# Kernel tuning notes

Hardware: AMD Instinct MI355X
Metric: run time of the kernel (lower is better)

## Reference

```python
import jax, jax.numpy as jnp
import numpy as np

DIM = 768
NUM_HEADS = 12
HEAD_DIM = DIM // NUM_HEADS
SCALE = HEAD_DIM ** -0.5


def setup_inputs() -> dict:
    key = jax.random.key(0)
    k1, k2, k3, k4 = jax.random.split(key, 4)
    B, N = 4, 2048
    x = jax.random.normal(k1, (B, N, DIM), dtype=jnp.float32)
    # torch Linear(dim, 3*dim, bias=False): weight [3*dim, dim]
    w_qkv = jax.random.normal(k2, (3 * DIM, DIM), dtype=jnp.float32) * (DIM ** -0.5)
    # proj: Linear(dim, dim) with bias
    w_proj = jax.random.normal(k3, (DIM, DIM), dtype=jnp.float32) * (DIM ** -0.5)
    b_proj = jax.random.normal(k4, (DIM,), dtype=jnp.float32) * 0.01
    return {"x": x, "w_qkv": w_qkv, "w_proj": w_proj, "b_proj": b_proj}


def reference(x, w_qkv, w_proj, b_proj):
    B, N, D = x.shape
    H, Hd = NUM_HEADS, HEAD_DIM
    qkv = x @ w_qkv.T                              # [B, N, 3D]
    qkv = qkv.reshape(B, N, 3, H, Hd)
    qkv = jnp.transpose(qkv, (2, 0, 3, 1, 4))      # [3, B, H, N, Hd]
    q, k, v = qkv[0], qkv[1], qkv[2]
    attn = jnp.einsum('bhnd,bhmd->bhnm', q, k) * SCALE  # [B, H, N, N]
    attn = jax.nn.softmax(attn, axis=-1)
    out = jnp.einsum('bhnm,bhmd->bhnd', attn, v)   # [B, H, N, Hd]
    out = jnp.transpose(out, (0, 2, 1, 3)).reshape(B, N, D)
    return out @ w_proj.T + b_proj
```

## Files before the change

kernel.cpp:

```cpp
#include <hip/hip_runtime.h>
#include <hip/hip_bf16.h>

#define DIM      768
#define NHEADS   12
#define HEADDIM  64
#define BATCH    4
#define SEQ      2048
#define NROWS    (BATCH * SEQ)
#define QKVCOLS  (3 * DIM)
#define SLOT     ((size_t)BATCH * NHEADS * SEQ * HEADDIM)

#define QSCALE_LOG2 0.18033688011112042f

typedef short bf16x8_t __attribute__((ext_vector_type(8)));
typedef short bf16x4_t __attribute__((ext_vector_type(4)));
typedef float f32x4_t  __attribute__((ext_vector_type(4)));

__device__ __forceinline__ short f2bf(float f) {
    union { __hip_bfloat16 h; short s; } u;
    u.h = __float2bfloat16(f);
    return u.s;
}

__device__ __forceinline__ float exp2_fast(float x) {
#if __has_builtin(__builtin_amdgcn_exp2f)
    return __builtin_amdgcn_exp2f(x);
#else
    return __expf(x * 0.6931471805599453f);
#endif
}

__device__ __forceinline__ void stage16(const __hip_bfloat16* g, __hip_bfloat16* l) {
    __builtin_amdgcn_global_load_lds(
        (const __attribute__((address_space(1))) void*)g,
        (__attribute__((address_space(3))) void*)l,
        16, 0, 0);
}

#define NX8  ((size_t)NROWS * DIM / 8)
#define NWQ8 ((size_t)QKVCOLS * DIM / 8)
#define NWP8 ((size_t)DIM * DIM / 8)

__global__ __launch_bounds__(256) void cvt_all(const float* __restrict__ X,
                                               const float* __restrict__ Wq,
                                               const float* __restrict__ Wp,
                                               __hip_bfloat16* __restrict__ Xb,
                                               __hip_bfloat16* __restrict__ Wqb,
                                               __hip_bfloat16* __restrict__ Wpb) {
    size_t i = (size_t)blockIdx.x * 256 + threadIdx.x;
    const float* src; __hip_bfloat16* dst; size_t off;
    if (i < NX8)                  { src = X;  dst = Xb;  off = i; }
    else if (i < NX8 + NWQ8)      { src = Wq; dst = Wqb; off = i - NX8; }
    else                          { src = Wp; dst = Wpb; off = i - NX8 - NWQ8; }
    float4 a = ((const float4*)src)[off * 2];
    float4 b = ((const float4*)src)[off * 2 + 1];
    bf16x8_t o;
    o[0] = f2bf(a.x); o[1] = f2bf(a.y); o[2] = f2bf(a.z); o[3] = f2bf(a.w);
    o[4] = f2bf(b.x); o[5] = f2bf(b.y); o[6] = f2bf(b.z); o[7] = f2bf(b.w);
    *(bf16x8_t*)(dst + off * 8) = o;
}

#define GEMM_CORE(Aptr, Bptr)                                                   \
    __shared__ __hip_bfloat16 As[128 * 64];                                     \
    __shared__ __hip_bfloat16 Bs[128 * 64];                                     \
    const int tid  = threadIdx.x;                                               \
    const int wave = tid >> 6;                                                  \
    const int lane = tid & 63;                                                  \
    const int quad = lane >> 4;                                                 \
    const int l16  = lane & 15;                                                 \
    const int wm   = wave >> 1;                                                 \
    const int wn   = wave & 1;                                                  \
    const int m0   = blockIdx.x * 128;                                          \
    const int n0   = blockIdx.y * 128;                                          \
    const int sr   = lane >> 3;                     \
    const int sc   = ((lane & 7) ^ sr) * 8;         \
    f32x4_t acc[4][4];                                                          \
    _Pragma("unroll")                                                           \
    for (int i = 0; i < 4; i++)                                                 \
        _Pragma("unroll")                                                       \
        for (int j = 0; j < 4; j++) acc[i][j] = (f32x4_t){0.f, 0.f, 0.f, 0.f};  \
    for (int k0 = 0; k0 < 768; k0 += 64) {                                      \
        __syncthreads();                                                        \
        _Pragma("unroll")                                                       \
        for (int i = 0; i < 4; i++) {                                           \
            int seg = wave * 4 + i;                                  \
            int row = seg * 8 + sr;                                             \
            stage16(Aptr + (size_t)(m0 + row) * 768 + k0 + sc, As + seg * 512); \
            stage16(Bptr + (size_t)(n0 + row) * 768 + k0 + sc, Bs + seg * 512); \
        }                                                                       \
        __syncthreads();               \
        _Pragma("unroll")                                                       \
        for (int kc = 0; kc < 2; kc++) {                                        \
            const int dsw = ((kc * 4 + quad) ^ (l16 & 7)) * 8;                  \
            bf16x8_t af[4], bfr[4];                                             \
            _Pragma("unroll")                                                   \
            for (int mt = 0; mt < 4; mt++)                                      \
                af[mt] = *(const bf16x8_t*)(As + (wm * 64 + mt * 16 + l16) * 64 + dsw); \
            _Pragma("unroll")                                                   \
            for (int nt = 0; nt < 4; nt++)                                      \
                bfr[nt] = *(const bf16x8_t*)(Bs + (wn * 64 + nt * 16 + l16) * 64 + dsw); \
            _Pragma("unroll")                                                   \
            for (int mt = 0; mt < 4; mt++)                                      \
                _Pragma("unroll")                                               \
                for (int nt = 0; nt < 4; nt++)                                  \
                    acc[mt][nt] = __builtin_amdgcn_mfma_f32_16x16x32_bf16(      \
                        af[mt], bfr[nt], acc[mt][nt], 0, 0, 0);                 \
        }                                                                       \
    }

__global__ __launch_bounds__(256) void qkv_gemm(const __hip_bfloat16* __restrict__ Wqb,
                                                const __hip_bfloat16* __restrict__ Xb,
                                                __hip_bfloat16* __restrict__ QKV) {
    GEMM_CORE(Wqb, Xb)

    const int bidx = n0 >> 11;
    const int nb   = (n0 & 2047) + wn * 64;
#pragma unroll
    for (int mt = 0; mt < 4; mt++) {
        int colbase = m0 + wm * 64 + mt * 16;
        int which   = colbase / 768;
        int rem     = colbase - which * 768;
        int h       = rem >> 6;
        int dbase   = (rem & 63) + quad * 4;
#pragma unroll
        for (int nt = 0; nt < 4; nt++) {
            int n = nb + nt * 16 + l16;
            if (which == 2) {
                size_t base = 2 * SLOT + (((size_t)bidx * NHEADS + h) * HEADDIM + dbase) * SEQ + n;
#pragma unroll
                for (int r = 0; r < 4; r++)
                    QKV[base + (size_t)r * SEQ] = __float2bfloat16(acc[mt][nt][r]);
            } else {
                float sc2 = (which == 0) ? QSCALE_LOG2 : 1.0f;
                size_t addr = (size_t)which * SLOT
                            + (((size_t)bidx * NHEADS + h) * SEQ + n) * HEADDIM + dbase;
                bf16x4_t pk;
#pragma unroll
                for (int r = 0; r < 4; r++) pk[r] = f2bf(acc[mt][nt][r] * sc2);
                *(bf16x4_t*)(QKV + addr) = pk;
            }
        }
    }
}

__global__ __launch_bounds__(512, 6) void attn(const __hip_bfloat16* __restrict__ QKV,
                                               __hip_bfloat16* __restrict__ ATT) {
    __shared__ __hip_bfloat16 lds[288 * 64];

    const int tid  = threadIdx.x;
    const int wave = tid >> 6;
    const int lane = tid & 63;
    const int quad = lane >> 4;
    const int l16  = lane & 15;
    const int qb   = blockIdx.x;
    const int bh   = blockIdx.y;
    const int b    = bh / NHEADS;
    const int h    = bh - b * NHEADS;

    const __hip_bfloat16* Qg = QKV + 0 * SLOT + (((size_t)b * NHEADS + h) * SEQ) * HEADDIM;
    const __hip_bfloat16* Kg = QKV + 1 * SLOT + (((size_t)b * NHEADS + h) * SEQ) * HEADDIM;
    const __hip_bfloat16* Vg = QKV + 2 * SLOT + (((size_t)b * NHEADS + h) * HEADDIM) * SEQ;

    const int rs = tid >> 3;
    const int es = (tid & 7) * 8;

#pragma unroll
    for (int i = 0; i < 2; i++) {
        int c = tid + i * 512;
        int r = c >> 3, e = (c & 7) * 8;
        *(bf16x8_t*)(lds + r * 72 + e) =
            *(const bf16x8_t*)(Qg + (size_t)(qb * 128 + r) * HEADDIM + e);
    }
    *(bf16x8_t*)(lds + 9216 + rs * 72 + es)  = *(const bf16x8_t*)(Kg + (size_t)rs * HEADDIM + es);
    *(bf16x8_t*)(lds + 13824 + rs * 72 + es) = *(const bf16x8_t*)(Vg + (size_t)rs * SEQ + es);
    __syncthreads();

    bf16x8_t aq[2];
#pragma unroll
    for (int kc = 0; kc < 2; kc++)
        aq[kc] = *(const bf16x8_t*)(lds + (wave * 16 + l16) * 72 + kc * 32 + quad * 8);
    __syncthreads();

    f32x4_t o[4];
#pragma unroll
    for (int dt = 0; dt < 4; dt++) o[dt] = (f32x4_t){0.f, 0.f, 0.f, 0.f};
    float l_part = 0.f;

    for (int t = 0; t < SEQ / 64; t++) {
        const int cur  = t & 1;
        const int boff = cur ? 0 : 9216;
        const __hip_bfloat16* Kc = lds + boff;
        const __hip_bfloat16* Vc = lds + boff + 4608;

        bf16x8_t nk, nv;
        const bool has_next = (t + 1 < SEQ / 64);
        if (has_next) {
            int nn0 = (t + 1) * 64;
            nk = *(const bf16x8_t*)(Kg + (size_t)(nn0 + rs) * HEADDIM + es);
            nv = *(const bf16x8_t*)(Vg + (size_t)rs * SEQ + nn0 + es);
        }

        f32x4_t s[4];
#pragma unroll
        for (int mt = 0; mt < 4; mt++) s[mt] = (f32x4_t){0.f, 0.f, 0.f, 0.f};
#pragma unroll
        for (int kc = 0; kc < 2; kc++) {
#pragma unroll
            for (int mt = 0; mt < 4; mt++) {
                bf16x8_t bk = *(const bf16x8_t*)(Kc + (mt * 16 + l16) * 72 + kc * 32 + quad * 8);
                s[mt] = __builtin_amdgcn_mfma_f32_16x16x32_bf16(bk, aq[kc], s[mt], 0, 0, 0);
            }
        }

#pragma unroll
        for (int mt = 0; mt < 4; mt++)
#pragma unroll
            for (int r = 0; r < 4; r++) {
                float p = exp2_fast(s[mt][r]);
                s[mt][r] = p;
                l_part += p;
            }

#pragma unroll
        for (int kb = 0; kb < 4; kb++) {
            bf16x4_t pb;
#pragma unroll
            for (int j = 0; j < 4; j++) pb[j] = f2bf(s[kb][j]);
#pragma unroll
            for (int dt = 0; dt < 4; dt++) {
                bf16x4_t av = *(const bf16x4_t*)(Vc + (dt * 16 + l16) * 72 + kb * 16 + quad * 4);
                o[dt] = __builtin_amdgcn_mfma_f32_16x16x16bf16_1k(av, pb, o[dt], 0, 0, 0);
            }
        }

        if (has_next) {
            const int aoff = cur ? 9216 : 0;
            *(bf16x8_t*)(lds + aoff + rs * 72 + es)        = nk;
            *(bf16x8_t*)(lds + aoff + 4608 + rs * 72 + es) = nv;
        }
        __syncthreads();
    }

    l_part += __shfl_xor(l_part, 16);
    l_part += __shfl_xor(l_part, 32);
    float inv = 1.f / l_part;

    const int n = qb * 128 + wave * 16 + l16;
    __hip_bfloat16* orow = ATT + ((size_t)b * SEQ + n) * DIM + h * HEADDIM + quad * 4;
#pragma unroll
    for (int dt = 0; dt < 4; dt++) {
        bf16x4_t pk;
#pragma unroll
        for (int r = 0; r < 4; r++) pk[r] = f2bf(o[dt][r] * inv);
        *(bf16x4_t*)(orow + dt * 16) = pk;
    }
}

__global__ __launch_bounds__(256) void proj_gemm(const __hip_bfloat16* __restrict__ A,
                                                 const __hip_bfloat16* __restrict__ B,
                                                 const float* __restrict__ bias,
                                                 float* __restrict__ OUT) {
    GEMM_CORE(A, B)

#pragma unroll
    for (int mt = 0; mt < 4; mt++) {
#pragma unroll
        for (int nt = 0; nt < 4; nt++) {
            int col = n0 + wn * 64 + nt * 16 + l16;
            float bv = bias[col];
#pragma unroll
            for (int r = 0; r < 4; r++) {
                int row = m0 + wm * 64 + mt * 16 + quad * 4 + r;
                OUT[(size_t)row * 768 + col] = acc[mt][nt][r] + bv;
            }
        }
    }
}

extern "C" void kernel_launch(void* const* d_in, const int* in_sizes, int n_in,
                              void* d_out, int out_size, void* d_ws, size_t ws_size,
                              hipStream_t stream) {
    const float* x      = (const float*)d_in[0];
    const float* w_qkv  = (const float*)d_in[1];
    const float* w_proj = (const float*)d_in[2];
    const float* b_proj = (const float*)d_in[3];
    float* out = (float*)d_out;

    __hip_bfloat16* qkv_ws = (__hip_bfloat16*)d_ws;
    __hip_bfloat16* xb     = qkv_ws + 3 * SLOT;
    __hip_bfloat16* att_ws = xb;
    __hip_bfloat16* wqb    = xb + (size_t)NROWS * DIM;
    __hip_bfloat16* wpb    = wqb + (size_t)QKVCOLS * DIM;

    int cvt_blocks = (int)((NX8 + NWQ8 + NWP8) / 256);
    cvt_all<<<cvt_blocks, 256, 0, stream>>>(x, w_qkv, w_proj, xb, wqb, wpb);

    dim3 g1(QKVCOLS / 128, NROWS / 128);
    qkv_gemm<<<g1, 256, 0, stream>>>(wqb, xb, qkv_ws);

    dim3 g2(SEQ / 128, BATCH * NHEADS);
    attn<<<g2, 512, 0, stream>>>(qkv_ws, att_ws);

    dim3 g3(NROWS / 128, DIM / 128);
    proj_gemm<<<g3, 256, 0, stream>>>(att_ws, wpb, b_proj, out);
}
```

Before: 237.7 us.

## Double-buffer GEMM LDS tiles and remap blocks to XCDs for L2 locality

```diff
diff --git a/kernel.cpp b/kernel.cpp
--- a/kernel.cpp
+++ b/kernel.cpp
@@ -61,8 +61,8 @@
 }
 
 #define GEMM_CORE(Aptr, Bptr)                                                   \
-    __shared__ __hip_bfloat16 As[128 * 64];                                     \
-    __shared__ __hip_bfloat16 Bs[128 * 64];                                     \
+    __shared__ __hip_bfloat16 As[2 * 128 * 32];                                 \
+    __shared__ __hip_bfloat16 Bs[2 * 128 * 32];                                 \
     const int tid  = threadIdx.x;                                               \
     const int wave = tid >> 6;                                                  \
     const int lane = tid & 63;                                                  \
@@ -70,47 +70,63 @@
     const int l16  = lane & 15;                                                 \
     const int wm   = wave >> 1;                                                 \
     const int wn   = wave & 1;                                                  \
-    const int m0   = blockIdx.x * 128;                                          \
-    const int n0   = blockIdx.y * 128;                                          \
-    const int sr   = lane >> 3;                     \
-    const int sc   = ((lane & 7) ^ sr) * 8;         \
+    const int m0   = bx * 128;                                                  \
+    const int n0   = by * 128;                                                  \
+    const int lr   = lane >> 2;                      \
+    const int lp   = ((lane & 3) ^ (lr & 3)) * 8;     \
     f32x4_t acc[4][4];                                                          \
     _Pragma("unroll")                                                           \
     for (int i = 0; i < 4; i++)                                                 \
         _Pragma("unroll")                                                       \
         for (int j = 0; j < 4; j++) acc[i][j] = (f32x4_t){0.f, 0.f, 0.f, 0.f};  \
-    for (int k0 = 0; k0 < 768; k0 += 64) {                                      \
-        __syncthreads();                                                        \
+    _Pragma("unroll")                                                           \
+    for (int i = 0; i < 2; i++) {                                               \
+        int seg = wave * 2 + i;                                       \
+        int row = seg * 16 + lr;                                                \
+        stage16(Aptr + (size_t)(m0 + row) * 768 + lp, As + seg * 512);          \
+        stage16(Bptr + (size_t)(n0 + row) * 768 + lp, Bs + seg * 512);          \
+    }                                                                           \
+    __syncthreads();                                                            \
+    for (int k0 = 0; k0 < 768; k0 += 32) {                                      \
+        const int cur = (k0 >> 5) & 1;                                          \
+        if (k0 + 32 < 768) {                                                    \
+            const int nxt = cur ^ 1;                                            \
+            _Pragma("unroll")                                                   \
+            for (int i = 0; i < 2; i++) {                                       \
+                int seg = wave * 2 + i;                                         \
+                int row = seg * 16 + lr;                                        \
+                stage16(Aptr + (size_t)(m0 + row) * 768 + k0 + 32 + lp,         \
+                        As + nxt * 4096 + seg * 512);                           \
+                stage16(Bptr + (size_t)(n0 + row) * 768 + k0 + 32 + lp,         \
+                        Bs + nxt * 4096 + seg * 512);                           \
+            }                                                                   \
+        }                                                                       \
+        const int dsw = ((quad ^ (l16 & 3)) * 8) + cur * 4096;                  \
+        bf16x8_t af[4], bfr[4];                                                 \
         _Pragma("unroll")                                                       \
-        for (int i = 0; i < 4; i++) {                                           \
-            int seg = wave * 4 + i;                                  \
-            int row = seg * 8 + sr;                                             \
-            stage16(Aptr + (size_t)(m0 + row) * 768 + k0 + sc, As + seg * 512); \
-            stage16(Bptr + (size_t)(n0 + row) * 768 + k0 + sc, Bs + seg * 512); \
-        }                                                                       \
-        __syncthreads();               \
+        for (int mt = 0; mt < 4; mt++)                                          \
+            af[mt] = *(const bf16x8_t*)(As + (wm * 64 + mt * 16 + l16) * 32 + dsw); \
         _Pragma("unroll")                                                       \
-        for (int kc = 0; kc < 2; kc++) {                                        \
-            const int dsw = ((kc * 4 + quad) ^ (l16 & 7)) * 8;                  \
-            bf16x8_t af[4], bfr[4];                                             \
-            _Pragma("unroll")                                                   \
-            for (int mt = 0; mt < 4; mt++)                                      \
-                af[mt] = *(const bf16x8_t*)(As + (wm * 64 + mt * 16 + l16) * 64 + dsw); \
+        for (int nt = 0; nt < 4; nt++)                                          \
+            bfr[nt] = *(const bf16x8_t*)(Bs + (wn * 64 + nt * 16 + l16) * 32 + dsw); \
+        _Pragma("unroll")                                                       \
+        for (int mt = 0; mt < 4; mt++)                                          \
             _Pragma("unroll")                                                   \
             for (int nt = 0; nt < 4; nt++)                                      \
-                bfr[nt] = *(const bf16x8_t*)(Bs + (wn * 64 + nt * 16 + l16) * 64 + dsw); \
-            _Pragma("unroll")                                                   \
-            for (int mt = 0; mt < 4; mt++)                                      \
-                _Pragma("unroll")                                               \
-                for (int nt = 0; nt < 4; nt++)                                  \
-                    acc[mt][nt] = __builtin_amdgcn_mfma_f32_16x16x32_bf16(      \
-                        af[mt], bfr[nt], acc[mt][nt], 0, 0, 0);                 \
-        }                                                                       \
+                acc[mt][nt] = __builtin_amdgcn_mfma_f32_16x16x32_bf16(          \
+                    af[mt], bfr[nt], acc[mt][nt], 0, 0, 0);                     \
+        __syncthreads();          \
     }
 
 __global__ __launch_bounds__(256) void qkv_gemm(const __hip_bfloat16* __restrict__ Wqb,
                                                 const __hip_bfloat16* __restrict__ Xb,
                                                 __hip_bfloat16* __restrict__ QKV) {
+    const int lin = blockIdx.y * 18 + blockIdx.x;
+    const int xcd = lin & 7;
+    const int idx = lin >> 3;
+    const int by  = xcd * 8 + idx / 18;
+    const int bx  = idx - (idx / 18) * 18;
+
     GEMM_CORE(Wqb, Xb)
 
     const int bidx = n0 >> 11;
@@ -152,10 +168,14 @@
     const int lane = tid & 63;
     const int quad = lane >> 4;
     const int l16  = lane & 15;
-    const int qb   = blockIdx.x;
-    const int bh   = blockIdx.y;
-    const int b    = bh / NHEADS;
-    const int h    = bh - b * NHEADS;
+
+    const int lin = blockIdx.y * 16 + blockIdx.x;
+    const int xcd = lin & 7;
+    const int idx = lin >> 3;
+    const int bh  = xcd * 6 + (idx >> 4);
+    const int qb  = idx & 15;
+    const int b   = bh / NHEADS;
+    const int h   = bh - b * NHEADS;
 
     const __hip_bfloat16* Qg = QKV + 0 * SLOT + (((size_t)b * NHEADS + h) * SEQ) * HEADDIM;
     const __hip_bfloat16* Kg = QKV + 1 * SLOT + (((size_t)b * NHEADS + h) * SEQ) * HEADDIM;
@@ -260,6 +280,9 @@
                                                  const __hip_bfloat16* __restrict__ B,
                                                  const float* __restrict__ bias,
                                                  float* __restrict__ OUT) {
+    const int bx = blockIdx.x;
+    const int by = blockIdx.y;
+
     GEMM_CORE(A, B)
 
 #pragma unroll
```

New measurement: 232.9 us. 2.0% less time.
